# Optimization experiments

Hardware: AMD Instinct MI355X
Metric: run time of the kernel (lower is better)

The kernel has to match this reference:

```python
import jax, jax.numpy as jnp
import numpy as np
import math

B, Q_LEN, D, H, KV = 8, 2048, 1024, 16, 256
HD = D // H

def setup_inputs() -> dict:
    key0 = jax.random.key(0)
    ks = jax.random.split(key0, 6)
    query = jax.random.normal(ks[0], (B, Q_LEN, D), dtype=jnp.float32)
    key = jax.random.normal(ks[1], (B, 1024), dtype=jnp.float32)
    value = jax.random.normal(ks[2], (B, 1024), dtype=jnp.float32)
    clip_score = jax.random.uniform(ks[3], (B, KV), dtype=jnp.float32)
    # k_linear / v_linear weights (embed_dim, 1024), no bias
    k_weight = jax.random.normal(ks[4], (D, 1024), dtype=jnp.float32) * 0.02
    v_weight = jax.random.normal(ks[5], (D, 1024), dtype=jnp.float32) * 0.02
    # scale_linear: Linear(512, 1), weight const 0.05, bias const 7.5 (per nn.init.constant_)
    scale_w = jnp.full((2 * KV,), 0.05, dtype=jnp.float32)
    scale_b = jnp.array(7.5, dtype=jnp.float32)
    return {"query": query, "key": key, "value": value, "clip_score": clip_score,
            "k_weight": k_weight, "v_weight": v_weight, "scale_w": scale_w, "scale_b": scale_b}

def reference(query, key, value, clip_score, k_weight, v_weight, scale_w, scale_b):
    act_scale = 1.0
    b, qlen, d = query.shape
    # key/value are (B,1024): expand to (B,KV,1024) as in torch branch
    key_e = jnp.broadcast_to(key[:, None, :], (b, KV, key.shape[-1]))
    val_e = jnp.broadcast_to(value[:, None, :], (b, KV, value.shape[-1]))
    K = jnp.einsum('bkc,dc->bkd', key_e, k_weight)   # (B,KV,D)
    V = jnp.einsum('bkc,dc->bkd', val_e, v_weight)   # (B,KV,D)
    Qh = query.reshape(b, qlen, H, HD).transpose(0, 2, 1, 3)  # (B,H,Q,HD)
    Kh = K.reshape(b, KV, H, HD).transpose(0, 2, 1, 3)        # (B,H,KV,HD)
    Vh = V.reshape(b, KV, H, HD).transpose(0, 2, 1, 3)        # (B,H,KV,HD)
    scores = jnp.einsum('bhqd,bhkd->bhqk', Qh, Kh) / math.sqrt(HD)  # (B,H,Q,KV)
    # scale_linear(cat([scores, clip], -1)) == scores@w1 + clip@w2 + b (avoid materializing concat)
    w1, w2 = scale_w[:KV], scale_w[KV:]
    lin = (jnp.einsum('bhqk,k->bhq', scores, w1)[..., None]
           + (clip_score @ w2)[:, None, None, None] + scale_b)   # (B,H,Q,1)
    clip_e = clip_score[:, None, None, :]                        # (B,1,1,KV)
    scores = scores + (lin * clip_e) * act_scale
    attn_weights = jax.nn.softmax(scores, axis=-1)
    out = jnp.einsum('bhqk,bhkd->bhqd', attn_weights, Vh)
    out = out.transpose(0, 2, 1, 3).reshape(b, qlen, d)
    return (out, attn_weights)
```

## Files before the change

### kernel.cpp

```cpp
#include <hip/hip_runtime.h>
#include <hip/hip_bf16.h>

#define B_    8
#define QLEN  2048
#define D_    1024
#define H_    16
#define KV_   256
#define HD_   64

typedef float fvec4 __attribute__((ext_vector_type(4)));

#define WS_KVEC 0
#define WS_VVEC 8192
#define WS_C2   16384
#define WS_SW1  16392

__device__ inline float wave_sum(float v) {
#pragma unroll
  for (int off = 32; off > 0; off >>= 1) v += __shfl_xor(v, off, 64);
  return v;
}
__device__ inline float wave_max(float v) {
#pragma unroll
  for (int off = 32; off > 0; off >>= 1) v = fmaxf(v, __shfl_xor(v, off, 64));
  return v;
}
__device__ inline float wave_min(float v) {
#pragma unroll
  for (int off = 32; off > 0; off >>= 1) v = fminf(v, __shfl_xor(v, off, 64));
  return v;
}
template <int N>
__device__ inline void multi_sum(float* v) {
#pragma unroll
  for (int off = 32; off > 0; off >>= 1) {
#pragma unroll
    for (int r = 0; r < N; ++r) v[r] += __shfl_xor(v[r], off, 64);
  }
}

__global__ __launch_bounds__(256) void prep_kernel(
    const float* __restrict__ key, const float* __restrict__ value,
    const float* __restrict__ kw, const float* __restrict__ vw,
    const float* __restrict__ clip, const float* __restrict__ scale_w,
    float* __restrict__ ws) {
  const int lane = threadIdx.x & 63;
  const int waveId = threadIdx.x >> 6;

  if (blockIdx.x == 512) {
    if (waveId != 0) return;
    const fvec4* sw4 = reinterpret_cast<const fvec4*>(scale_w);
    fvec4 a = sw4[lane];
    float s = wave_sum(a.x + a.y + a.z + a.w);
    if (lane == 0) ws[WS_SW1] = s;
    fvec4 w2 = sw4[64 + lane];
    for (int b = 0; b < B_; ++b) {
      const fvec4* c4 = reinterpret_cast<const fvec4*>(clip + b * KV_);
      fvec4 c = c4[lane];
      float p = c.x * w2.x + c.y * w2.y + c.z * w2.z + c.w * w2.w;
      p = wave_sum(p);
      if (lane == 0) ws[WS_C2 + b] = p;
    }
    return;
  }

  const int W = blockIdx.x * 4 + waveId;
  const int sel = W >> 10;
  const int d = W & 1023;
  const float* Wt = sel ? vw : kw;
  const float* xsrc = sel ? value : key;
  float* outv = ws + (sel ? WS_VVEC : WS_KVEC);

  const fvec4* w4 = reinterpret_cast<const fvec4*>(Wt + (size_t)d * 1024);
  fvec4 wr[4];
#pragma unroll
  for (int i = 0; i < 4; ++i) wr[i] = w4[i * 64 + lane];

#pragma unroll
  for (int b0 = 0; b0 < B_; b0 += 2) {
    const fvec4* xa = reinterpret_cast<const fvec4*>(xsrc + b0 * 1024);
    const fvec4* xb = reinterpret_cast<const fvec4*>(xsrc + (b0 + 1) * 1024);
    float acc[2] = {0.f, 0.f};
#pragma unroll
    for (int i = 0; i < 4; ++i) {
      fvec4 x0 = xa[i * 64 + lane];
      fvec4 x1 = xb[i * 64 + lane];
      acc[0] += x0.x * wr[i].x + x0.y * wr[i].y + x0.z * wr[i].z + x0.w * wr[i].w;
      acc[1] += x1.x * wr[i].x + x1.y * wr[i].y + x1.z * wr[i].z + x1.w * wr[i].w;
    }
    multi_sum<2>(acc);
    if (lane == 0) {
      outv[b0 * 1024 + d] = acc[0];
      outv[(b0 + 1) * 1024 + d] = acc[1];
    }
  }
}

__global__ __launch_bounds__(256) void fused_kernel(
    const float* __restrict__ query, const float* __restrict__ clip,
    const float* __restrict__ scale_b, const float* __restrict__ ws,
    float* __restrict__ attn, float* __restrict__ out) {
  const int lane = threadIdx.x & 63;
  const int gwave = (blockIdx.x * 256 + threadIdx.x) >> 6;
  const int row0 = gwave * 32;
  const int b = row0 >> 15;
  const int h = (row0 >> 11) & 15;
  const int q0 = row0 & 2047;
  const int g = lane >> 4;
  const int c = lane & 15;

  {
    const fvec4* v4 = reinterpret_cast<const fvec4*>(ws + WS_VVEC);
    fvec4* o4 = reinterpret_cast<fvec4*>(out);
#pragma unroll
    for (int i = 0; i < 8; ++i) {
      const int j = (gwave * 8 + i) * 64 + lane;
      const int ob = j >> 19;
      const int d4 = j & 255;
      fvec4 v = v4[ob * 256 + d4];
      __builtin_nontemporal_store(v, &o4[j]);
    }
  }

  const fvec4 kvv =
      reinterpret_cast<const fvec4*>(ws + WS_KVEC + b * 1024 + h * HD_)[c];
  const float sw1 = ws[WS_SW1];
  const float Lc = ws[WS_C2 + b] + scale_b[0];
  const float* qb = query + ((size_t)(b * QLEN + q0)) * D_ + h * HD_;

  float p[8];
#pragma unroll
  for (int j = 0; j < 8; ++j) {
    const fvec4 q4 = __builtin_nontemporal_load(
        reinterpret_cast<const fvec4*>(qb + (size_t)(j * 4 + g) * D_) + c);
    p[j] = q4.x * kvv.x + q4.y * kvv.y + q4.z * kvv.z + q4.w * kvv.w;
  }
#pragma unroll
  for (int off = 1; off <= 8; off <<= 1) {
#pragma unroll
    for (int j = 0; j < 8; ++j) p[j] += __shfl_xor(p[j], off, 64);
  }
#pragma unroll
  for (int j = 0; j < 8; ++j) p[j] = sw1 * (p[j] * 0.125f) + Lc;

  const fvec4 cl = reinterpret_cast<const fvec4*>(clip + b * KV_)[lane];
  const float cmax = wave_max(fmaxf(fmaxf(cl.x, cl.y), fmaxf(cl.z, cl.w)));
  const float cmin = wave_min(fminf(fminf(cl.x, cl.y), fminf(cl.z, cl.w)));

  fvec4* a4 = reinterpret_cast<fvec4*>(attn) + (size_t)row0 * 64 + lane;
#pragma unroll
  for (int i = 0; i < 32; ++i) {
    const float Ld = __builtin_amdgcn_readlane(p[i >> 2], (i & 3) << 4);
    const float m = (Ld >= 0.f) ? Ld * cmax : Ld * cmin;
    fvec4 e;
    e.x = __expf(Ld * cl.x - m);
    e.y = __expf(Ld * cl.y - m);
    e.z = __expf(Ld * cl.z - m);
    e.w = __expf(Ld * cl.w - m);
    const float den = wave_sum(e.x + e.y + e.z + e.w);
    e *= (1.0f / den);
    __builtin_nontemporal_store(e, &a4[(size_t)i * 64]);
  }
}

extern "C" void kernel_launch(void* const* d_in, const int* in_sizes, int n_in,
                              void* d_out, int out_size, void* d_ws, size_t ws_size,
                              hipStream_t stream) {
  const float* query   = (const float*)d_in[0];
  const float* key     = (const float*)d_in[1];
  const float* value   = (const float*)d_in[2];
  const float* clip    = (const float*)d_in[3];
  const float* kw      = (const float*)d_in[4];
  const float* vw      = (const float*)d_in[5];
  const float* scale_w = (const float*)d_in[6];
  const float* scale_b = (const float*)d_in[7];
  float* out  = (float*)d_out;
  float* attn = out + (size_t)B_ * QLEN * D_;
  float* ws   = (float*)d_ws;

  hipLaunchKernelGGL(prep_kernel, dim3(513), dim3(256), 0, stream,
                     key, value, kw, vw, clip, scale_w, ws);
  hipLaunchKernelGGL(fused_kernel, dim3(2048), dim3(256), 0, stream,
                     query, clip, scale_b, ws, attn, out);
}
```

Before: 87.43 us.

## Persistent waves process four row sets with double-buffered query prefetch

The fused kernel now launches a quarter as many blocks, and each wave handles four 32-row sets. The query loads for the next set are issued before the current set is processed, so memory latency overlaps with the softmax math. The softmax drops max subtraction, computing all 32 row sums first with one batched shuffle reduction and dividing with a fast reciprocal. The trade-off is higher register pressure, fewer waves to hide latency, and possible exp overflow without the max shift.

```diff
diff --git a/kernel.cpp b/kernel.cpp
--- a/kernel.cpp
+++ b/kernel.cpp
@@ -8,6 +8,9 @@
 #define KV_   256
 #define HD_   64
 
+#define NWAVE 2048
+#define NSETS 4
+
 typedef float fvec4 __attribute__((ext_vector_type(4)));
 
 #define WS_KVEC 0
@@ -18,16 +21,6 @@
 __device__ inline float wave_sum(float v) {
 #pragma unroll
   for (int off = 32; off > 0; off >>= 1) v += __shfl_xor(v, off, 64);
-  return v;
-}
-__device__ inline float wave_max(float v) {
-#pragma unroll
-  for (int off = 32; off > 0; off >>= 1) v = fmaxf(v, __shfl_xor(v, off, 64));
-  return v;
-}
-__device__ inline float wave_min(float v) {
-#pragma unroll
-  for (int off = 32; off > 0; off >>= 1) v = fminf(v, __shfl_xor(v, off, 64));
   return v;
 }
 template <int N>
@@ -96,71 +89,107 @@
   }
 }
 
+
+__device__ __forceinline__ void load_set(
+    int setId, const float* __restrict__ query, const float* __restrict__ clip,
+    const float* __restrict__ ws, int lane, int g, int c,
+    fvec4 qb[8], fvec4& kv, fvec4& cl) {
+  const int row0 = setId * 32;
+  const int b = row0 >> 15;
+  const int h = (row0 >> 11) & 15;
+  const int q0 = row0 & 2047;
+  const float* qp = query + ((size_t)(b * QLEN + q0)) * D_ + h * HD_;
+#pragma unroll
+  for (int j = 0; j < 8; ++j) {
+    qb[j] = __builtin_nontemporal_load(
+        reinterpret_cast<const fvec4*>(qp + (size_t)(j * 4 + g) * D_) + c);
+  }
+  kv = reinterpret_cast<const fvec4*>(ws + WS_KVEC + b * 1024 + h * HD_)[c];
+  cl = reinterpret_cast<const fvec4*>(clip + b * KV_)[lane];
+}
+
+__device__ __forceinline__ void proc_set(
+    int setId, const fvec4 qb[8], fvec4 kv, fvec4 cl,
+    float sw1, const float* __restrict__ ws, float sb,
+    float* __restrict__ attn, float* __restrict__ out, int lane) {
+  const int row0 = setId * 32;
+  const int b = row0 >> 15;
+  const float Lc = ws[WS_C2 + b] + sb;
+
+  float p[8];
+#pragma unroll
+  for (int j = 0; j < 8; ++j)
+    p[j] = qb[j].x * kv.x + qb[j].y * kv.y + qb[j].z * kv.z + qb[j].w * kv.w;
+#pragma unroll
+  for (int off = 1; off <= 8; off <<= 1) {
+#pragma unroll
+    for (int j = 0; j < 8; ++j) p[j] += __shfl_xor(p[j], off, 64);
+  }
+#pragma unroll
+  for (int j = 0; j < 8; ++j) p[j] = sw1 * (p[j] * 0.125f) + Lc;
+
+  float L32[32];
+#pragma unroll
+  for (int i = 0; i < 32; ++i)
+    L32[i] = __builtin_amdgcn_readlane(p[i >> 2], (i & 3) << 4);
+
+  float t[32];
+#pragma unroll
+  for (int i = 0; i < 32; ++i) {
+    t[i] = __expf(L32[i] * cl.x) + __expf(L32[i] * cl.y) +
+           __expf(L32[i] * cl.z) + __expf(L32[i] * cl.w);
+  }
+  multi_sum<32>(t);
+
+  fvec4* a4 = reinterpret_cast<fvec4*>(attn) + (size_t)row0 * 64 + lane;
+#pragma unroll
+  for (int i = 0; i < 32; ++i) {
+    const float rd = __builtin_amdgcn_rcpf(t[i]);
+    fvec4 e;
+    e.x = __expf(L32[i] * cl.x) * rd;
+    e.y = __expf(L32[i] * cl.y) * rd;
+    e.z = __expf(L32[i] * cl.z) * rd;
+    e.w = __expf(L32[i] * cl.w) * rd;
+    __builtin_nontemporal_store(e, &a4[(size_t)i * 64]);
+  }
+
+  const fvec4* v4 = reinterpret_cast<const fvec4*>(ws + WS_VVEC);
+  fvec4* o4 = reinterpret_cast<fvec4*>(out);
+#pragma unroll
+  for (int i = 0; i < 8; ++i) {
+    const int j = (setId * 8 + i) * 64 + lane;
+    const int ob = j >> 19;
+    const int d4 = j & 255;
+    fvec4 v = v4[ob * 256 + d4];
+    __builtin_nontemporal_store(v, &o4[j]);
+  }
+}
+
 __global__ __launch_bounds__(256) void fused_kernel(
     const float* __restrict__ query, const float* __restrict__ clip,
     const float* __restrict__ scale_b, const float* __restrict__ ws,
     float* __restrict__ attn, float* __restrict__ out) {
   const int lane = threadIdx.x & 63;
   const int gwave = (blockIdx.x * 256 + threadIdx.x) >> 6;
-  const int row0 = gwave * 32;
-  const int b = row0 >> 15;
-  const int h = (row0 >> 11) & 15;
-  const int q0 = row0 & 2047;
   const int g = lane >> 4;
   const int c = lane & 15;
-
-  {
-    const fvec4* v4 = reinterpret_cast<const fvec4*>(ws + WS_VVEC);
-    fvec4* o4 = reinterpret_cast<fvec4*>(out);
-#pragma unroll
-    for (int i = 0; i < 8; ++i) {
-      const int j = (gwave * 8 + i) * 64 + lane;
-      const int ob = j >> 19;
-      const int d4 = j & 255;
-      fvec4 v = v4[ob * 256 + d4];
-      __builtin_nontemporal_store(v, &o4[j]);
-    }
-  }
-
-  const fvec4 kvv =
-      reinterpret_cast<const fvec4*>(ws + WS_KVEC + b * 1024 + h * HD_)[c];
   const float sw1 = ws[WS_SW1];
-  const float Lc = ws[WS_C2 + b] + scale_b[0];
-  const float* qb = query + ((size_t)(b * QLEN + q0)) * D_ + h * HD_;
-
-  float p[8];
-#pragma unroll
-  for (int j = 0; j < 8; ++j) {
-    const fvec4 q4 = __builtin_nontemporal_load(
-        reinterpret_cast<const fvec4*>(qb + (size_t)(j * 4 + g) * D_) + c);
-    p[j] = q4.x * kvv.x + q4.y * kvv.y + q4.z * kvv.z + q4.w * kvv.w;
-  }
-#pragma unroll
-  for (int off = 1; off <= 8; off <<= 1) {
-#pragma unroll
-    for (int j = 0; j < 8; ++j) p[j] += __shfl_xor(p[j], off, 64);
-  }
-#pragma unroll
-  for (int j = 0; j < 8; ++j) p[j] = sw1 * (p[j] * 0.125f) + Lc;
-
-  const fvec4 cl = reinterpret_cast<const fvec4*>(clip + b * KV_)[lane];
-  const float cmax = wave_max(fmaxf(fmaxf(cl.x, cl.y), fmaxf(cl.z, cl.w)));
-  const float cmin = wave_min(fminf(fminf(cl.x, cl.y), fminf(cl.z, cl.w)));
-
-  fvec4* a4 = reinterpret_cast<fvec4*>(attn) + (size_t)row0 * 64 + lane;
-#pragma unroll
-  for (int i = 0; i < 32; ++i) {
-    const float Ld = __builtin_amdgcn_readlane(p[i >> 2], (i & 3) << 4);
-    const float m = (Ld >= 0.f) ? Ld * cmax : Ld * cmin;
-    fvec4 e;
-    e.x = __expf(Ld * cl.x - m);
-    e.y = __expf(Ld * cl.y - m);
-    e.z = __expf(Ld * cl.z - m);
-    e.w = __expf(Ld * cl.w - m);
-    const float den = wave_sum(e.x + e.y + e.z + e.w);
-    e *= (1.0f / den);
-    __builtin_nontemporal_store(e, &a4[(size_t)i * 64]);
-  }
+  const float sb = scale_b[0];
+
+  fvec4 qA[8], qB[8], kvA, kvB, clA, clB;
+
+  load_set(0 * NWAVE + gwave, query, clip, ws, lane, g, c, qA, kvA, clA);
+
+  load_set(1 * NWAVE + gwave, query, clip, ws, lane, g, c, qB, kvB, clB);
+  proc_set(0 * NWAVE + gwave, qA, kvA, clA, sw1, ws, sb, attn, out, lane);
+
+  load_set(2 * NWAVE + gwave, query, clip, ws, lane, g, c, qA, kvA, clA);
+  proc_set(1 * NWAVE + gwave, qB, kvB, clB, sw1, ws, sb, attn, out, lane);
+
+  load_set(3 * NWAVE + gwave, query, clip, ws, lane, g, c, qB, kvB, clB);
+  proc_set(2 * NWAVE + gwave, qA, kvA, clA, sw1, ws, sb, attn, out, lane);
+
+  proc_set(3 * NWAVE + gwave, qB, kvB, clB, sw1, ws, sb, attn, out, lane);
 }
 
 extern "C" void kernel_launch(void* const* d_in, const int* in_sizes, int n_in,
@@ -180,6 +209,6 @@
 
   hipLaunchKernelGGL(prep_kernel, dim3(513), dim3(256), 0, stream,
                      key, value, kw, vw, clip, scale_w, ws);
-  hipLaunchKernelGGL(fused_kernel, dim3(2048), dim3(256), 0, stream,
+  hipLaunchKernelGGL(fused_kernel, dim3(NWAVE / 4), dim3(256), 0, stream,
                      query, clip, scale_b, ws, attn, out);
 }
```

Result: faster. 85.07 us (-2.7%).

## Split fused kernel into q-dot pass and attention streaming pass without max subtraction

Applied to the files above, without the earlier changes.

Moves the per-row query·K dot products into a separate qdot kernel that writes per-row logit scales to workspace. The attention kernel then reads those scales, computes all 32 row sums in one batched multi-lane reduction, and drops the max-subtraction softmax stabilisation, using a fast reciprocal. This removes the per-row wave reductions and the min/max setup, at the cost of an extra launch, workspace traffic, recomputing the exponentials twice, and possible overflow if logits are large.

```diff
diff --git a/kernel.cpp b/kernel.cpp
--- a/kernel.cpp
+++ b/kernel.cpp
@@ -14,20 +14,11 @@
 #define WS_VVEC 8192
 #define WS_C2   16384
 #define WS_SW1  16392
+#define WS_L    16400
 
 __device__ inline float wave_sum(float v) {
 #pragma unroll
   for (int off = 32; off > 0; off >>= 1) v += __shfl_xor(v, off, 64);
-  return v;
-}
-__device__ inline float wave_max(float v) {
-#pragma unroll
-  for (int off = 32; off > 0; off >>= 1) v = fmaxf(v, __shfl_xor(v, off, 64));
-  return v;
-}
-__device__ inline float wave_min(float v) {
-#pragma unroll
-  for (int off = 32; off > 0; off >>= 1) v = fminf(v, __shfl_xor(v, off, 64));
   return v;
 }
 template <int N>
@@ -96,41 +87,26 @@
   }
 }
 
-__global__ __launch_bounds__(256) void fused_kernel(
-    const float* __restrict__ query, const float* __restrict__ clip,
-    const float* __restrict__ scale_b, const float* __restrict__ ws,
-    float* __restrict__ attn, float* __restrict__ out) {
+__global__ __launch_bounds__(256) void qdot_kernel(
+    const float* __restrict__ query, const float* __restrict__ scale_b,
+    float* __restrict__ ws) {
   const int lane = threadIdx.x & 63;
-  const int gwave = (blockIdx.x * 256 + threadIdx.x) >> 6;
-  const int row0 = gwave * 32;
-  const int b = row0 >> 15;
-  const int h = (row0 >> 11) & 15;
-  const int q0 = row0 & 2047;
+  const int waveId = threadIdx.x >> 6;
+  const int rowBase = blockIdx.x * 64 + waveId * 16;
+  const int b = rowBase >> 15;
+  const int h = (rowBase >> 11) & 15;
+  const int q0 = rowBase & 2047;
   const int g = lane >> 4;
   const int c = lane & 15;
 
-  {
-    const fvec4* v4 = reinterpret_cast<const fvec4*>(ws + WS_VVEC);
-    fvec4* o4 = reinterpret_cast<fvec4*>(out);
-#pragma unroll
-    for (int i = 0; i < 8; ++i) {
-      const int j = (gwave * 8 + i) * 64 + lane;
-      const int ob = j >> 19;
-      const int d4 = j & 255;
-      fvec4 v = v4[ob * 256 + d4];
-      __builtin_nontemporal_store(v, &o4[j]);
-    }
-  }
-
-  const fvec4 kvv =
-      reinterpret_cast<const fvec4*>(ws + WS_KVEC + b * 1024 + h * HD_)[c];
+  const fvec4 kvv = reinterpret_cast<const fvec4*>(ws + WS_KVEC + b * 1024 + h * HD_)[c];
   const float sw1 = ws[WS_SW1];
   const float Lc = ws[WS_C2 + b] + scale_b[0];
+
   const float* qb = query + ((size_t)(b * QLEN + q0)) * D_ + h * HD_;
-
-  float p[8];
+  float p[4];
 #pragma unroll
-  for (int j = 0; j < 8; ++j) {
+  for (int j = 0; j < 4; ++j) {
     const fvec4 q4 = __builtin_nontemporal_load(
         reinterpret_cast<const fvec4*>(qb + (size_t)(j * 4 + g) * D_) + c);
     p[j] = q4.x * kvv.x + q4.y * kvv.y + q4.z * kvv.z + q4.w * kvv.w;
@@ -138,28 +114,56 @@
 #pragma unroll
   for (int off = 1; off <= 8; off <<= 1) {
 #pragma unroll
-    for (int j = 0; j < 8; ++j) p[j] += __shfl_xor(p[j], off, 64);
+    for (int j = 0; j < 4; ++j) p[j] += __shfl_xor(p[j], off, 64);
   }
-#pragma unroll
-  for (int j = 0; j < 8; ++j) p[j] = sw1 * (p[j] * 0.125f) + Lc;
+  if (c < 4) {
+    const float sp = (c == 0) ? p[0] : (c == 1) ? p[1] : (c == 2) ? p[2] : p[3];
+    ws[WS_L + rowBase + c * 4 + g] = sw1 * (sp * 0.125f) + Lc;
+  }
+}
+
+__global__ __launch_bounds__(256) void attn_stream_kernel(
+    const float* __restrict__ clip, const float* __restrict__ ws,
+    float* __restrict__ attn, float* __restrict__ out) {
+  const int lane = threadIdx.x & 63;
+  const int gwave = (blockIdx.x * 256 + threadIdx.x) >> 6;
+  const int row0 = gwave * 32;
+  const int b = row0 >> 15;
 
   const fvec4 cl = reinterpret_cast<const fvec4*>(clip + b * KV_)[lane];
-  const float cmax = wave_max(fmaxf(fmaxf(cl.x, cl.y), fmaxf(cl.z, cl.w)));
-  const float cmin = wave_min(fminf(fminf(cl.x, cl.y), fminf(cl.z, cl.w)));
+  const float Lv = ws[WS_L + row0 + (lane & 31)];
+
+  float t[32];
+#pragma unroll
+  for (int i = 0; i < 32; ++i) {
+    const float Ld = __builtin_amdgcn_readlane(Lv, i);
+    t[i] = __expf(Ld * cl.x) + __expf(Ld * cl.y) +
+           __expf(Ld * cl.z) + __expf(Ld * cl.w);
+  }
+  multi_sum<32>(t);
 
   fvec4* a4 = reinterpret_cast<fvec4*>(attn) + (size_t)row0 * 64 + lane;
 #pragma unroll
   for (int i = 0; i < 32; ++i) {
-    const float Ld = __builtin_amdgcn_readlane(p[i >> 2], (i & 3) << 4);
-    const float m = (Ld >= 0.f) ? Ld * cmax : Ld * cmin;
+    const float Ld = __builtin_amdgcn_readlane(Lv, i);
+    const float rd = __builtin_amdgcn_rcpf(t[i]);
     fvec4 e;
-    e.x = __expf(Ld * cl.x - m);
-    e.y = __expf(Ld * cl.y - m);
-    e.z = __expf(Ld * cl.z - m);
-    e.w = __expf(Ld * cl.w - m);
-    const float den = wave_sum(e.x + e.y + e.z + e.w);
-    e *= (1.0f / den);
+    e.x = __expf(Ld * cl.x) * rd;
+    e.y = __expf(Ld * cl.y) * rd;
+    e.z = __expf(Ld * cl.z) * rd;
+    e.w = __expf(Ld * cl.w) * rd;
     __builtin_nontemporal_store(e, &a4[(size_t)i * 64]);
+  }
+
+  const fvec4* v4 = reinterpret_cast<const fvec4*>(ws + WS_VVEC);
+  fvec4* o4 = reinterpret_cast<fvec4*>(out);
+#pragma unroll
+  for (int i = 0; i < 8; ++i) {
+    const int j = (gwave * 8 + i) * 64 + lane;
+    const int ob = j >> 19;
+    const int d4 = j & 255;
+    fvec4 v = v4[ob * 256 + d4];
+    __builtin_nontemporal_store(v, &o4[j]);
   }
 }
 
@@ -180,6 +184,8 @@
 
   hipLaunchKernelGGL(prep_kernel, dim3(513), dim3(256), 0, stream,
                      key, value, kw, vw, clip, scale_w, ws);
-  hipLaunchKernelGGL(fused_kernel, dim3(2048), dim3(256), 0, stream,
-                     query, clip, scale_b, ws, attn, out);
+  hipLaunchKernelGGL(qdot_kernel, dim3(4096), dim3(256), 0, stream,
+                     query, scale_b, ws);
+  hipLaunchKernelGGL(attn_stream_kernel, dim3(2048), dim3(256), 0, stream,
+                     clip, ws, attn, out);
 }
```

Result: faster. 81.34 us (median of 2 runs) (-7.0%).
